# Optimization experiments

Hardware: AMD Instinct MI355X
Metric: run time of the kernel (lower is better)

The kernel has to match this reference:

```python
import math
import jax, jax.numpy as jnp
import numpy as np

BSZ, SEQ, DIM = 2, 2048, 4096
N_HEADS, N_KV = 32, 8
HEAD_DIM = DIM // N_HEADS  # 128
N_REP = N_HEADS // N_KV    # 4
EPS = 1e-5
ROPE_THETA = 500000.0


def setup_inputs() -> dict:
    key = jax.random.key(0)
    ks = jax.random.split(key, 6)
    scale = 0.02
    x = jax.random.normal(ks[0], (BSZ, SEQ, DIM), dtype=jnp.float32)
    wq = jax.random.normal(ks[1], (N_HEADS * HEAD_DIM, DIM), dtype=jnp.float32) * scale
    wk = jax.random.normal(ks[2], (N_KV * HEAD_DIM, DIM), dtype=jnp.float32) * scale
    wv = jax.random.normal(ks[3], (N_KV * HEAD_DIM, DIM), dtype=jnp.float32) * scale
    wo = jax.random.normal(ks[4], (N_HEADS * HEAD_DIM, DIM), dtype=jnp.float32).T * scale  # [DIM, n_heads*hd] -> stored as [out,in]
    wo = jax.random.normal(ks[4], (DIM, N_HEADS * HEAD_DIM), dtype=jnp.float32) * scale
    # RoPE tables (real/imag parts of freqs_cis)
    inv_freq = 1.0 / (ROPE_THETA ** (jnp.arange(0, HEAD_DIM, 2, dtype=jnp.float32) / HEAD_DIM))
    angles = jnp.arange(SEQ, dtype=jnp.float32)[:, None] * inv_freq[None, :]  # [SEQ, HEAD_DIM//2]
    cos, sin = jnp.cos(angles), jnp.sin(angles)
    # causal additive mask
    neg_inf = jnp.finfo(jnp.float32).min
    mask = jnp.where(jnp.tril(jnp.ones((SEQ, SEQ), dtype=bool)), 0.0, neg_inf).astype(jnp.float32)
    return {"x": x, "wq": wq, "wk": wk, "wv": wv, "wo": wo,
            "cos": cos, "sin": sin, "mask": mask, "start_pos": 0}


def _apply_rope(t, cos, sin):
    # t: [b, s, h, hd]; pairs (even, odd) as in view_as_complex
    tf = t.astype(jnp.float32).reshape(*t.shape[:-1], HEAD_DIM // 2, 2)
    e, o = tf[..., 0], tf[..., 1]
    c = cos[None, :, None, :]
    s = sin[None, :, None, :]
    out = jnp.stack([e * c - o * s, e * s + o * c], axis=-1)
    return out.reshape(t.shape).astype(t.dtype)


def _rmsnorm(t):
    tf = t.astype(jnp.float32)
    return (tf * jax.lax.rsqrt(jnp.mean(tf * tf, axis=-1, keepdims=True) + EPS)).astype(t.dtype)


def reference(x, wq, wk, wv, wo, cos, sin, mask, start_pos):
    b, s, _ = x.shape
    xq = (x @ wq.T).reshape(b, s, N_HEADS, HEAD_DIM)
    xk = (x @ wk.T).reshape(b, s, N_KV, HEAD_DIM)
    xv = (x @ wv.T).reshape(b, s, N_KV, HEAD_DIM)
    xq = _apply_rope(xq, cos, sin)
    xk = _apply_rope(xk, cos, sin)
    xq = _rmsnorm(xq)
    xk = _rmsnorm(xk)
    # KV cache write/read with start_pos=0 over seqlen tokens is identity here.
    # GQA without repeat_interleave: q head h attends kv head h // N_REP
    q = xq.transpose(0, 2, 1, 3).reshape(b, N_KV, N_REP, s, HEAD_DIM)
    k = xk.transpose(0, 2, 1, 3)  # [b, n_kv, s, hd]
    v = xv.transpose(0, 2, 1, 3)
    scale = 1.0 / math.sqrt(HEAD_DIM)
    scores = jnp.einsum('bgrqd,bgkd->bgrqk', q, k) * scale + mask[None, None, None]
    probs = jax.nn.softmax(scores, axis=-1)
    out = jnp.einsum('bgrqk,bgkd->bgrqd', probs, v)
    out = out.reshape(b, N_HEADS, s, HEAD_DIM).transpose(0, 2, 1, 3).reshape(b, s, N_HEADS * HEAD_DIM)
    return out @ wo.T
```

## Files before the change

### kernel.cpp

```cpp
#include <hip/hip_runtime.h>
#include <hip/hip_bf16.h>
#include <stdint.h>

#define SEQ 2048
#define DIMSZ 4096
#define QKVN 6144

typedef __attribute__((ext_vector_type(8))) __bf16 bf16x8;
typedef __attribute__((ext_vector_type(4))) float f32x4;

static __device__ __forceinline__ void gld_lds16(const void* g, void* l) {
  __builtin_amdgcn_global_load_lds(
      (__attribute__((address_space(1))) void*)(g),
      (__attribute__((address_space(3))) void*)(l), 16, 0, 0);
}

__global__ __launch_bounds__(256) void k_cvt(const float* __restrict__ in,
                                             __bf16* __restrict__ out, long n) {
  long i = (long)blockIdx.x * 256 + threadIdx.x;
  long stride = (long)gridDim.x * 256;
  for (long e = i * 8; e < n; e += stride * 8) {
    float4 v0 = *(const float4*)(in + e);
    float4 v1 = *(const float4*)(in + e + 4);
    bf16x8 o;
    o[0] = (__bf16)v0.x; o[1] = (__bf16)v0.y; o[2] = (__bf16)v0.z; o[3] = (__bf16)v0.w;
    o[4] = (__bf16)v1.x; o[5] = (__bf16)v1.y; o[6] = (__bf16)v1.z; o[7] = (__bf16)v1.w;
    *(bf16x8*)(out + e) = o;
  }
}

template <typename OutT>
__global__ __launch_bounds__(512, 2) void k_gemm256(const __bf16* __restrict__ A,
                                                    const __bf16* __restrict__ B,
                                                    OutT* __restrict__ C,
                                                    int M, int N, int K) {
  __shared__ __bf16 As[2][256 * 64];
  __shared__ __bf16 Bs[2][256 * 64];
  const int t = threadIdx.x;
  const int l = t & 63;
  const int w = t >> 6;
  const int wm = w >> 2;
  const int wn = w & 3;
  const int lr = l & 15, lg = l >> 4;
  const int sw = lr & 7;
  const int bm = blockIdx.y, bn = blockIdx.x;

  const __bf16* Ab = A + (size_t)bm * 256 * K;
  const __bf16* Bb = B + (size_t)bn * 256 * K;

  const int srow = t >> 3;
  const int scol = ((t & 7) ^ (srow & 7)) << 3;
  const int ldst = (t & ~63) * 8;
  const __bf16* Asrc = Ab + (size_t)srow * K + scol;
  const __bf16* Bsrc = Bb + (size_t)srow * K + scol;

#define STAGE_TILE(buf, kt)                                             \
  do {                                                                  \
    _Pragma("unroll") for (int i_ = 0; i_ < 4; ++i_)                    \
        gld_lds16(Asrc + (size_t)(i_ * 64) * K + (kt), &As[buf][i_ * 4096 + ldst]); \
    _Pragma("unroll") for (int i_ = 0; i_ < 4; ++i_)                    \
        gld_lds16(Bsrc + (size_t)(i_ * 64) * K + (kt), &Bs[buf][i_ * 4096 + ldst]); \
  } while (0)

  f32x4 acc[8][4] = {};
  bf16x8 a[4][2], b[2][2];

  const int nt = K >> 6;

  STAGE_TILE(0, 0);
  __syncthreads();

  for (int tI = 0; tI < nt; ++tI) {
    const int cur = tI & 1;

#pragma unroll
    for (int mi = 0; mi < 4; ++mi)
#pragma unroll
      for (int kk = 0; kk < 2; ++kk)
        a[mi][kk] = *(const bf16x8*)&As[cur][(wm * 128 + mi * 16 + lr) * 64 + (((kk * 4 + lg) ^ sw) * 8)];
#pragma unroll
    for (int ni = 0; ni < 2; ++ni)
#pragma unroll
      for (int kk = 0; kk < 2; ++kk)
        b[ni][kk] = *(const bf16x8*)&Bs[cur][(wn * 64 + ni * 16 + lr) * 64 + (((kk * 4 + lg) ^ sw) * 8)];
    if (tI + 1 < nt) STAGE_TILE(cur ^ 1, (size_t)(tI + 1) * 64);
    __builtin_amdgcn_s_barrier();
    __builtin_amdgcn_s_setprio(1);
#pragma unroll
    for (int mi = 0; mi < 4; ++mi)
#pragma unroll
      for (int ni = 0; ni < 2; ++ni)
#pragma unroll
        for (int kk = 0; kk < 2; ++kk)
          acc[mi][ni] = __builtin_amdgcn_mfma_f32_16x16x32_bf16(a[mi][kk], b[ni][kk], acc[mi][ni], 0, 0, 0);
    __builtin_amdgcn_s_setprio(0);

#pragma unroll
    for (int ni = 0; ni < 2; ++ni)
#pragma unroll
      for (int kk = 0; kk < 2; ++kk)
        b[ni][kk] = *(const bf16x8*)&Bs[cur][(wn * 64 + (ni + 2) * 16 + lr) * 64 + (((kk * 4 + lg) ^ sw) * 8)];
    __builtin_amdgcn_s_barrier();
    __builtin_amdgcn_s_setprio(1);
#pragma unroll
    for (int mi = 0; mi < 4; ++mi)
#pragma unroll
      for (int ni = 0; ni < 2; ++ni)
#pragma unroll
        for (int kk = 0; kk < 2; ++kk)
          acc[mi][ni + 2] = __builtin_amdgcn_mfma_f32_16x16x32_bf16(a[mi][kk], b[ni][kk], acc[mi][ni + 2], 0, 0, 0);
    __builtin_amdgcn_s_setprio(0);

#pragma unroll
    for (int mi = 0; mi < 4; ++mi)
#pragma unroll
      for (int kk = 0; kk < 2; ++kk)
        a[mi][kk] = *(const bf16x8*)&As[cur][(wm * 128 + (mi + 4) * 16 + lr) * 64 + (((kk * 4 + lg) ^ sw) * 8)];
    __builtin_amdgcn_s_barrier();
    __builtin_amdgcn_s_setprio(1);
#pragma unroll
    for (int mi = 0; mi < 4; ++mi)
#pragma unroll
      for (int ni = 0; ni < 2; ++ni)
#pragma unroll
        for (int kk = 0; kk < 2; ++kk)
          acc[mi + 4][ni + 2] = __builtin_amdgcn_mfma_f32_16x16x32_bf16(a[mi][kk], b[ni][kk], acc[mi + 4][ni + 2], 0, 0, 0);
    __builtin_amdgcn_s_setprio(0);

#pragma unroll
    for (int ni = 0; ni < 2; ++ni)
#pragma unroll
      for (int kk = 0; kk < 2; ++kk)
        b[ni][kk] = *(const bf16x8*)&Bs[cur][(wn * 64 + ni * 16 + lr) * 64 + (((kk * 4 + lg) ^ sw) * 8)];
    __builtin_amdgcn_s_barrier();
    __builtin_amdgcn_s_setprio(1);
#pragma unroll
    for (int mi = 0; mi < 4; ++mi)
#pragma unroll
      for (int ni = 0; ni < 2; ++ni)
#pragma unroll
        for (int kk = 0; kk < 2; ++kk)
          acc[mi + 4][ni] = __builtin_amdgcn_mfma_f32_16x16x32_bf16(a[mi][kk], b[ni][kk], acc[mi + 4][ni], 0, 0, 0);
    __builtin_amdgcn_s_setprio(0);

    asm volatile("s_waitcnt vmcnt(0)" ::: "memory");
    __builtin_amdgcn_sched_barrier(0);
    __builtin_amdgcn_s_barrier();
  }
#undef STAGE_TILE

  const int row0 = bm * 256 + wm * 128;
  const int col0 = bn * 256 + wn * 64;
#pragma unroll
  for (int mi = 0; mi < 8; ++mi)
#pragma unroll
    for (int ni = 0; ni < 4; ++ni)
#pragma unroll
      for (int r = 0; r < 4; ++r)
        C[(size_t)(row0 + mi * 16 + lg * 4 + r) * N + (col0 + ni * 16 + lr)] =
            (OutT)acc[mi][ni][r];
}

__global__ __launch_bounds__(256) void k_rope_norm(__bf16* __restrict__ qkv,
                                                   const float* __restrict__ cosT,
                                                   const float* __restrict__ sinT) {
  const int task = blockIdx.x * 4 + (threadIdx.x >> 6);
  const int l = threadIdx.x & 63;
  const int m = task / 40;
  const int h = task - m * 40;
  const int s = m & (SEQ - 1);
  const bool isQ = h < 32;
  const int col = isQ ? h * 128 : 4096 + (h - 32) * 128;
  __bf16* p = qkv + (size_t)m * QKVN + col + l * 2;
  float e = (float)p[0], o = (float)p[1];
  float c = cosT[s * 64 + l], sn = sinT[s * 64 + l];
  float e2 = e * c - o * sn;
  float o2 = e * sn + o * c;
  float ss = e2 * e2 + o2 * o2;
#pragma unroll
  for (int off = 32; off > 0; off >>= 1) ss += __shfl_xor(ss, off);
  float r = rsqrtf(ss * (1.0f / 128.0f) + 1e-5f);
  if (isQ) r *= 0.08838834764831845f;
  p[0] = (__bf16)(e2 * r);
  p[1] = (__bf16)(o2 * r);
}

__global__ __launch_bounds__(256) void k_transpose_v(const __bf16* __restrict__ qkv,
                                                     __bf16* __restrict__ vt) {
  __shared__ __bf16 tile[64][136];
  const int t = threadIdx.x;
  const int st = blockIdx.x, bg = blockIdx.y;
  const int b = bg >> 3, g = bg & 7;
  const int s0 = st * 64;
#pragma unroll
  for (int p = 0; p < 4; ++p) {
    int row = p * 16 + (t >> 4);
    int co = (t & 15) * 8;
    *(bf16x8*)&tile[row][co] =
        *(const bf16x8*)&qkv[(size_t)(b * SEQ + s0 + row) * QKVN + 5120 + g * 128 + co];
  }
  __syncthreads();
#pragma unroll
  for (int p = 0; p < 4; ++p) {
    int d = p * 32 + (t >> 3);
    int so = (t & 7) * 8;
    bf16x8 v;
#pragma unroll
    for (int j = 0; j < 8; ++j) v[j] = tile[so + j][d];
    *(bf16x8*)&vt[((size_t)bg * 128 + d) * SEQ + s0 + so] = v;
  }
}

__global__ __launch_bounds__(256) void k_flash(const __bf16* __restrict__ qkv,
                                               const __bf16* __restrict__ vt,
                                               __bf16* __restrict__ attno) {
  __shared__ __bf16 Ks[64 * 128];
  __shared__ __bf16 Vs[128 * 64];
  __shared__ __bf16 Ps[4][16 * 64];
  const int t = threadIdx.x, w = t >> 6, l = t & 63;
  const int lr = l & 15, lg = l >> 4;
  const int bh = blockIdx.y;
  const int b = bh >> 5, h = bh & 31, g = h >> 2;
  const int qt0 = blockIdx.x, qt1 = 31 - (int)blockIdx.x;

  const __bf16* Kb = qkv + 4096 + (size_t)(b * SEQ) * QKVN + g * 128;
  const __bf16* Vtb = vt + ((size_t)(b * 8 + g)) * 128 * SEQ;
  const int wbase = (t & ~63) * 8;
  const int sw = lr & 7;

  for (int pass = 0; pass < 2; ++pass) {
    const int qt = (pass == 0) ? qt0 : qt1;

    const __bf16* Qb = qkv + (size_t)(b * SEQ + qt * 64 + w * 16 + lr) * QKVN + h * 128;
    bf16x8 qf[4];
#pragma unroll
    for (int kk = 0; kk < 4; ++kk) qf[kk] = *(const bf16x8*)&Qb[kk * 32 + lg * 8];

    f32x4 oacc[8] = {};
    float mrow[4], lsum[4];
#pragma unroll
    for (int r = 0; r < 4; ++r) { mrow[r] = -1e30f; lsum[r] = 0.f; }

    for (int kt = 0; kt <= qt; ++kt) {
      const int kv0 = kt * 64;
#pragma unroll
      for (int i = 0; i < 4; ++i) {
        int e = i * 256 + t;
        gld_lds16(Kb + (size_t)(kv0 + (e >> 4)) * QKVN + ((e & 15) ^ ((e >> 4) & 7)) * 8,
                  &Ks[i * 2048 + wbase]);
      }
#pragma unroll
      for (int i = 0; i < 4; ++i) {
        int e = i * 256 + t;
        gld_lds16(Vtb + (size_t)(e >> 3) * SEQ + kv0 + (((e & 7) ^ ((e >> 3) & 7))) * 8,
                  &Vs[i * 2048 + wbase]);
      }
      __syncthreads();

      f32x4 sc[4] = {};
#pragma unroll
      for (int kk = 0; kk < 4; ++kk)
#pragma unroll
        for (int n = 0; n < 4; ++n) {
          bf16x8 kf = *(const bf16x8*)&Ks[(n * 16 + lr) * 128 + ((kk * 4 + lg) ^ sw) * 8];
          sc[n] = __builtin_amdgcn_mfma_f32_16x16x32_bf16(qf[kk], kf, sc[n], 0, 0, 0);
        }

      if (kt == qt) {
#pragma unroll
        for (int n = 0; n < 4; ++n)
#pragma unroll
          for (int r = 0; r < 4; ++r)
            if (n * 16 + lr > w * 16 + lg * 4 + r) sc[n][r] = -1e30f;
      }

#pragma unroll
      for (int r = 0; r < 4; ++r) {
        float pm = fmaxf(fmaxf(sc[0][r], sc[1][r]), fmaxf(sc[2][r], sc[3][r]));
#pragma unroll
        for (int off = 8; off > 0; off >>= 1) pm = fmaxf(pm, __shfl_xor(pm, off));
        float mn = fmaxf(mrow[r], pm);
        float corr = __expf(mrow[r] - mn);
        mrow[r] = mn;
        float ps = 0.f;
#pragma unroll
        for (int n = 0; n < 4; ++n) { sc[n][r] = __expf(sc[n][r] - mn); ps += sc[n][r]; }
#pragma unroll
        for (int off = 8; off > 0; off >>= 1) ps += __shfl_xor(ps, off);
        lsum[r] = lsum[r] * corr + ps;
#pragma unroll
        for (int dn = 0; dn < 8; ++dn) oacc[dn][r] *= corr;
      }

#pragma unroll
      for (int n = 0; n < 4; ++n)
#pragma unroll
        for (int r = 0; r < 4; ++r) {
          int row = lg * 4 + r;
          Ps[w][row * 64 + (((n * 2 + (lr >> 3)) ^ (row & 7)) * 8) + (lr & 7)] = (__bf16)sc[n][r];
        }

#pragma unroll
      for (int ks = 0; ks < 2; ++ks) {
        bf16x8 pf = *(const bf16x8*)&Ps[w][lr * 64 + ((ks * 4 + lg) ^ sw) * 8];
#pragma unroll
        for (int dn = 0; dn < 8; ++dn) {
          bf16x8 vf = *(const bf16x8*)&Vs[(dn * 16 + lr) * 64 + ((ks * 4 + lg) ^ sw) * 8];
          oacc[dn] = __builtin_amdgcn_mfma_f32_16x16x32_bf16(pf, vf, oacc[dn], 0, 0, 0);
        }
      }
      __syncthreads();
    }

    __bf16* Ob = attno + (size_t)(b * SEQ + qt * 64 + w * 16) * DIMSZ + h * 128;
#pragma unroll
    for (int dn = 0; dn < 8; ++dn)
#pragma unroll
      for (int r = 0; r < 4; ++r)
        Ob[(size_t)(lg * 4 + r) * DIMSZ + dn * 16 + lr] = (__bf16)(oacc[dn][r] / lsum[r]);
  }
}

extern "C" void kernel_launch(void* const* d_in, const int* in_sizes, int n_in,
                              void* d_out, int out_size, void* d_ws, size_t ws_size,
                              hipStream_t stream) {
  const float* x    = (const float*)d_in[0];
  const float* wq   = (const float*)d_in[1];
  const float* wk   = (const float*)d_in[2];
  const float* wv   = (const float*)d_in[3];
  const float* wo   = (const float*)d_in[4];
  const float* cosT = (const float*)d_in[5];
  const float* sinT = (const float*)d_in[6];

  char* ws = (char*)d_ws;
  __bf16* xb    = (__bf16*)(ws);
  __bf16* wqkvb = (__bf16*)(ws + 33554432);
  __bf16* qkvb  = (__bf16*)(ws + 83886080);
  __bf16* wob   = (__bf16*)(ws + 134217728);
  __bf16* vt    = (__bf16*)(ws + 167772160);
  __bf16* attno = (__bf16*)(ws + 176160768);
  float* out = (float*)d_out;

  k_cvt<<<8192, 256, 0, stream>>>(x, xb, 16777216L);
  k_cvt<<<8192, 256, 0, stream>>>(wq, wqkvb, 16777216L);
  k_cvt<<<2048, 256, 0, stream>>>(wk, wqkvb + 16777216, 4194304L);
  k_cvt<<<2048, 256, 0, stream>>>(wv, wqkvb + 20971520, 4194304L);
  k_cvt<<<8192, 256, 0, stream>>>(wo, wob, 16777216L);

  k_gemm256<__bf16><<<dim3(24, 16), 512, 0, stream>>>(xb, wqkvb, qkvb, 4096, QKVN, 4096);
  k_rope_norm<<<40960, 256, 0, stream>>>(qkvb, cosT, sinT);
  k_transpose_v<<<dim3(32, 16), 256, 0, stream>>>(qkvb, vt);
  k_flash<<<dim3(16, 64), 256, 0, stream>>>(qkvb, vt, attno);
  k_gemm256<float><<<dim3(16, 16), 512, 0, stream>>>(attno, wob, out, 4096, DIMSZ, 4096);
}
```

Measured before the change: 625.9 us.

## Split GEMM LDS stages into half-tiles and prefetch A two tiles ahead

Restructures the 256x256 bf16 GEMM main loop so the A and B tiles are split into 128-row halves. B halves are staged one tile ahead, interleaved between MFMA phases, and A is prefetched two k-tiles ahead into the buffer just consumed. The full vmcnt(0) drain at the end of each iteration becomes vmcnt(4), so loads stay in flight across iterations. It also drops the min-2-blocks launch bound and adds compiler memory fences around barriers, which may change register allocation and occupancy.

```diff
diff --git a/kernel.cpp b/kernel.cpp
--- a/kernel.cpp
+++ b/kernel.cpp
@@ -13,6 +13,12 @@
   __builtin_amdgcn_global_load_lds(
       (__attribute__((address_space(1))) void*)(g),
       (__attribute__((address_space(3))) void*)(l), 16, 0, 0);
+}
+
+static __device__ __forceinline__ void blockbar() {
+  asm volatile("" ::: "memory");
+  __builtin_amdgcn_s_barrier();
+  asm volatile("" ::: "memory");
 }
 
 __global__ __launch_bounds__(256) void k_cvt(const float* __restrict__ in,
@@ -30,12 +36,12 @@
 }
 
 template <typename OutT>
-__global__ __launch_bounds__(512, 2) void k_gemm256(const __bf16* __restrict__ A,
-                                                    const __bf16* __restrict__ B,
-                                                    OutT* __restrict__ C,
-                                                    int M, int N, int K) {
-  __shared__ __bf16 As[2][256 * 64];
-  __shared__ __bf16 Bs[2][256 * 64];
+__global__ __launch_bounds__(512) void k_gemm256(const __bf16* __restrict__ A,
+                                                 const __bf16* __restrict__ B,
+                                                 OutT* __restrict__ C,
+                                                 int M, int N, int K) {
+  __shared__ __align__(16) __bf16 As[2][2][128 * 64];
+  __shared__ __align__(16) __bf16 Bs[2][2][128 * 64];
   const int t = threadIdx.x;
   const int l = t & 63;
   const int w = t >> 6;
@@ -45,46 +51,87 @@
   const int sw = lr & 7;
   const int bm = blockIdx.y, bn = blockIdx.x;
 
-  const __bf16* Ab = A + (size_t)bm * 256 * K;
-  const __bf16* Bb = B + (size_t)bn * 256 * K;
-
   const int srow = t >> 3;
   const int scol = ((t & 7) ^ (srow & 7)) << 3;
-  const int ldst = (t & ~63) * 8;
-  const __bf16* Asrc = Ab + (size_t)srow * K + scol;
-  const __bf16* Bsrc = Bb + (size_t)srow * K + scol;
-
-#define STAGE_TILE(buf, kt)                                             \
-  do {                                                                  \
-    _Pragma("unroll") for (int i_ = 0; i_ < 4; ++i_)                    \
-        gld_lds16(Asrc + (size_t)(i_ * 64) * K + (kt), &As[buf][i_ * 4096 + ldst]); \
-    _Pragma("unroll") for (int i_ = 0; i_ < 4; ++i_)                    \
-        gld_lds16(Bsrc + (size_t)(i_ * 64) * K + (kt), &Bs[buf][i_ * 4096 + ldst]); \
+  const __bf16* pa0 = A + (size_t)(bm * 256 +   0 + srow) * K + scol;
+  const __bf16* pa1 = A + (size_t)(bm * 256 +  64 + srow) * K + scol;
+  const __bf16* pa2 = A + (size_t)(bm * 256 + 128 + srow) * K + scol;
+  const __bf16* pa3 = A + (size_t)(bm * 256 + 192 + srow) * K + scol;
+  const __bf16* pb0 = B + (size_t)(bn * 256 +   0 + srow) * K + scol;
+  const __bf16* pb1 = B + (size_t)(bn * 256 +  64 + srow) * K + scol;
+  const __bf16* pb2 = B + (size_t)(bn * 256 + 128 + srow) * K + scol;
+  const __bf16* pb3 = B + (size_t)(bn * 256 + 192 + srow) * K + scol;
+  const int ldst = t * 8;
+
+#define STAGE_A(buf, kc)                              \
+  do {                                                \
+    gld_lds16(pa0 + (kc), &As[buf][0][ldst]);         \
+    gld_lds16(pa1 + (kc), &As[buf][0][4096 + ldst]);  \
+    gld_lds16(pa2 + (kc), &As[buf][1][ldst]);         \
+    gld_lds16(pa3 + (kc), &As[buf][1][4096 + ldst]);  \
   } while (0)
+#define STAGE_B0(buf, kc)                             \
+  do {                                                \
+    gld_lds16(pb0 + (kc), &Bs[buf][0][ldst]);         \
+    gld_lds16(pb1 + (kc), &Bs[buf][0][4096 + ldst]);  \
+  } while (0)
+#define STAGE_B1(buf, kc)                             \
+  do {                                                \
+    gld_lds16(pb2 + (kc), &Bs[buf][1][ldst]);         \
+    gld_lds16(pb3 + (kc), &Bs[buf][1][4096 + ldst]);  \
+  } while (0)
+
+  const int c0 = ((lg ^ sw) * 8);
+  const int c1 = (((lg ^ sw) ^ 4) * 8);
+  const int aRow = lr;
+  const int bRow = (wn & 1) * 64 + lr;
 
   f32x4 acc[8][4] = {};
-  bf16x8 a[4][2], b[2][2];
-
   const int nt = K >> 6;
 
-  STAGE_TILE(0, 0);
-  __syncthreads();
-
-  for (int tI = 0; tI < nt; ++tI) {
-    const int cur = tI & 1;
-
+  STAGE_A(0, 0);
+  STAGE_B0(0, 0);
+  STAGE_B1(0, 0);
+  STAGE_A(1, (nt > 1 ? 64 : 0));
+  asm volatile("s_waitcnt vmcnt(4)" ::: "memory");
+  blockbar();
+
+  for (int T = 0; T < nt; ++T) {
+    const int cur = T & 1;
+    const int kB = (T + 1 < nt ? T + 1 : nt - 1) << 6;
+    const int kA = (T + 2 < nt ? T + 2 : nt - 1) << 6;
+    bf16x8 a[4][2], b0[2][2], b1[2][2];
+
+#pragma unroll
+    for (int mi = 0; mi < 4; ++mi) {
+      a[mi][0] = *(const bf16x8*)&As[cur][wm][(mi * 16 + aRow) * 64 + c0];
+      a[mi][1] = *(const bf16x8*)&As[cur][wm][(mi * 16 + aRow) * 64 + c1];
+    }
+#pragma unroll
+    for (int ni = 0; ni < 2; ++ni) {
+      b0[ni][0] = *(const bf16x8*)&Bs[cur][wn >> 1][(ni * 16 + bRow) * 64 + c0];
+      b0[ni][1] = *(const bf16x8*)&Bs[cur][wn >> 1][(ni * 16 + bRow) * 64 + c1];
+    }
+    STAGE_B0((T + 1) & 1, kB);
+    blockbar();
+    __builtin_amdgcn_s_setprio(1);
 #pragma unroll
     for (int mi = 0; mi < 4; ++mi)
 #pragma unroll
-      for (int kk = 0; kk < 2; ++kk)
-        a[mi][kk] = *(const bf16x8*)&As[cur][(wm * 128 + mi * 16 + lr) * 64 + (((kk * 4 + lg) ^ sw) * 8)];
-#pragma unroll
-    for (int ni = 0; ni < 2; ++ni)
-#pragma unroll
-      for (int kk = 0; kk < 2; ++kk)
-        b[ni][kk] = *(const bf16x8*)&Bs[cur][(wn * 64 + ni * 16 + lr) * 64 + (((kk * 4 + lg) ^ sw) * 8)];
-    if (tI + 1 < nt) STAGE_TILE(cur ^ 1, (size_t)(tI + 1) * 64);
-    __builtin_amdgcn_s_barrier();
+      for (int ni = 0; ni < 2; ++ni)
+#pragma unroll
+        for (int kk = 0; kk < 2; ++kk)
+          acc[mi][ni] = __builtin_amdgcn_mfma_f32_16x16x32_bf16(a[mi][kk], b0[ni][kk], acc[mi][ni], 0, 0, 0);
+    __builtin_amdgcn_s_setprio(0);
+    blockbar();
+
+#pragma unroll
+    for (int ni = 0; ni < 2; ++ni) {
+      b1[ni][0] = *(const bf16x8*)&Bs[cur][wn >> 1][((ni + 2) * 16 + bRow) * 64 + c0];
+      b1[ni][1] = *(const bf16x8*)&Bs[cur][wn >> 1][((ni + 2) * 16 + bRow) * 64 + c1];
+    }
+    STAGE_B1((T + 1) & 1, kB);
+    blockbar();
     __builtin_amdgcn_s_setprio(1);
 #pragma unroll
     for (int mi = 0; mi < 4; ++mi)
@@ -92,15 +139,16 @@
       for (int ni = 0; ni < 2; ++ni)
 #pragma unroll
         for (int kk = 0; kk < 2; ++kk)
-          acc[mi][ni] = __builtin_amdgcn_mfma_f32_16x16x32_bf16(a[mi][kk], b[ni][kk], acc[mi][ni], 0, 0, 0);
+          acc[mi][ni + 2] = __builtin_amdgcn_mfma_f32_16x16x32_bf16(a[mi][kk], b1[ni][kk], acc[mi][ni + 2], 0, 0, 0);
     __builtin_amdgcn_s_setprio(0);
-
-#pragma unroll
-    for (int ni = 0; ni < 2; ++ni)
-#pragma unroll
-      for (int kk = 0; kk < 2; ++kk)
-        b[ni][kk] = *(const bf16x8*)&Bs[cur][(wn * 64 + (ni + 2) * 16 + lr) * 64 + (((kk * 4 + lg) ^ sw) * 8)];
-    __builtin_amdgcn_s_barrier();
+    blockbar();
+
+#pragma unroll
+    for (int mi = 0; mi < 4; ++mi) {
+      a[mi][0] = *(const bf16x8*)&As[cur][wm][((mi + 4) * 16 + aRow) * 64 + c0];
+      a[mi][1] = *(const bf16x8*)&As[cur][wm][((mi + 4) * 16 + aRow) * 64 + c1];
+    }
+    blockbar();
     __builtin_amdgcn_s_setprio(1);
 #pragma unroll
     for (int mi = 0; mi < 4; ++mi)
@@ -108,46 +156,27 @@
       for (int ni = 0; ni < 2; ++ni)
 #pragma unroll
         for (int kk = 0; kk < 2; ++kk)
-          acc[mi][ni + 2] = __builtin_amdgcn_mfma_f32_16x16x32_bf16(a[mi][kk], b[ni][kk], acc[mi][ni + 2], 0, 0, 0);
+          acc[mi + 4][ni + 2] = __builtin_amdgcn_mfma_f32_16x16x32_bf16(a[mi][kk], b1[ni][kk], acc[mi + 4][ni + 2], 0, 0, 0);
     __builtin_amdgcn_s_setprio(0);
-
+    blockbar();
+
+    STAGE_A(cur, kA);
+    blockbar();
+    __builtin_amdgcn_s_setprio(1);
 #pragma unroll
     for (int mi = 0; mi < 4; ++mi)
 #pragma unroll
-      for (int kk = 0; kk < 2; ++kk)
-        a[mi][kk] = *(const bf16x8*)&As[cur][(wm * 128 + (mi + 4) * 16 + lr) * 64 + (((kk * 4 + lg) ^ sw) * 8)];
-    __builtin_amdgcn_s_barrier();
-    __builtin_amdgcn_s_setprio(1);
-#pragma unroll
-    for (int mi = 0; mi < 4; ++mi)
-#pragma unroll
       for (int ni = 0; ni < 2; ++ni)
 #pragma unroll
         for (int kk = 0; kk < 2; ++kk)
-          acc[mi + 4][ni + 2] = __builtin_amdgcn_mfma_f32_16x16x32_bf16(a[mi][kk], b[ni][kk], acc[mi + 4][ni + 2], 0, 0, 0);
+          acc[mi + 4][ni] = __builtin_amdgcn_mfma_f32_16x16x32_bf16(a[mi][kk], b0[ni][kk], acc[mi + 4][ni], 0, 0, 0);
     __builtin_amdgcn_s_setprio(0);
-
-#pragma unroll
-    for (int ni = 0; ni < 2; ++ni)
-#pragma unroll
-      for (int kk = 0; kk < 2; ++kk)
-        b[ni][kk] = *(const bf16x8*)&Bs[cur][(wn * 64 + ni * 16 + lr) * 64 + (((kk * 4 + lg) ^ sw) * 8)];
-    __builtin_amdgcn_s_barrier();
-    __builtin_amdgcn_s_setprio(1);
-#pragma unroll
-    for (int mi = 0; mi < 4; ++mi)
-#pragma unroll
-      for (int ni = 0; ni < 2; ++ni)
-#pragma unroll
-        for (int kk = 0; kk < 2; ++kk)
-          acc[mi + 4][ni] = __builtin_amdgcn_mfma_f32_16x16x32_bf16(a[mi][kk], b[ni][kk], acc[mi + 4][ni], 0, 0, 0);
-    __builtin_amdgcn_s_setprio(0);
-
-    asm volatile("s_waitcnt vmcnt(0)" ::: "memory");
-    __builtin_amdgcn_sched_barrier(0);
-    __builtin_amdgcn_s_barrier();
-  }
-#undef STAGE_TILE
+    asm volatile("s_waitcnt vmcnt(4)" ::: "memory");
+    blockbar();
+  }
+#undef STAGE_A
+#undef STAGE_B0
+#undef STAGE_B1
 
   const int row0 = bm * 256 + wm * 128;
   const int col0 = bn * 256 + wn * 64;
```

Result: no change. 631.0 us (+0.8%).
